# Kernel tuning notes

Hardware: AMD Instinct MI355X
Metric: run time of the kernel (lower is better)

The kernel has to match this reference:

```python
import jax, jax.numpy as jnp
import numpy as np

D_MODEL = 2048
N_HEADS = 16
HEAD_DIM = D_MODEL // N_HEADS
SCALE = HEAD_DIM ** -0.5
LN_EPS = 1e-5
N_LAYERS = 24


def _layernorm(x, g, b):
    mu = jnp.mean(x, axis=-1, keepdims=True)
    var = jnp.mean(jnp.square(x - mu), axis=-1, keepdims=True)
    return (x - mu) * jax.lax.rsqrt(var + LN_EPS) * g + b


def _split_heads(x):  # [B,S,D] -> [B,H,S,hd]
    B, S, _ = x.shape
    return x.reshape(B, S, N_HEADS, HEAD_DIM).transpose(0, 2, 1, 3)


def setup_inputs() -> dict:
    key = jax.random.key(0)
    ks = jax.random.split(key, 12)
    B, St, Si = 2, 2048, 1024
    std_qkv = D_MODEL ** -0.5
    std_o = (2 * N_LAYERS) ** -0.5
    return {
        "q_text": jax.random.normal(ks[0], (B, St, D_MODEL), jnp.float32),
        "q_image": jax.random.normal(ks[1], (B, Si, D_MODEL), jnp.float32),
        "k_text": jax.random.normal(ks[2], (B, St, D_MODEL), jnp.float32),
        "k_image": jax.random.normal(ks[3], (B, Si, D_MODEL), jnp.float32),
        "Wq": jax.random.normal(ks[4], (D_MODEL, D_MODEL), jnp.float32) * std_qkv,
        "Wk": jax.random.normal(ks[5], (D_MODEL, D_MODEL), jnp.float32) * std_qkv,
        "Wv": jax.random.normal(ks[6], (D_MODEL, D_MODEL), jnp.float32) * std_qkv,
        "Wo": jax.random.normal(ks[7], (D_MODEL, D_MODEL), jnp.float32) * std_o,
        "ln_text_g": jnp.ones((D_MODEL,), jnp.float32),
        "ln_text_b": jnp.zeros((D_MODEL,), jnp.float32),
        "ln_image_g": jnp.ones((D_MODEL,), jnp.float32),
        "ln_image_b": jnp.zeros((D_MODEL,), jnp.float32),
    }


def reference(q_text, q_image, k_text, k_image, Wq, Wk, Wv, Wo,
              ln_text_g, ln_text_b, ln_image_g, ln_image_b):
    # Normalize each key modality once, project to K/V, concat along seq.
    kt = _layernorm(k_text, ln_text_g, ln_text_b)
    ki = _layernorm(k_image, ln_image_g, ln_image_b)
    concat_k = jnp.concatenate([_split_heads(kt @ Wk.T), _split_heads(ki @ Wk.T)], axis=2)
    concat_v = jnp.concatenate([_split_heads(kt @ Wv.T), _split_heads(ki @ Wv.T)], axis=2)

    def attend(q, g, b):
        B, S, _ = q.shape
        qn = _layernorm(q, g, b)
        qh = _split_heads(qn @ Wq.T) * SCALE            # [B,H,Sq,hd]
        scores = jnp.einsum('bhqd,bhkd->bhqk', qh, concat_k)
        attn = jax.nn.softmax(scores.astype(jnp.float32), axis=-1).astype(q.dtype)
        out = jnp.einsum('bhqk,bhkd->bhqd', attn, concat_v)
        out = out.transpose(0, 2, 1, 3).reshape(B, S, D_MODEL)
        return out @ Wo.T

    out_text = attend(q_text, ln_text_g, ln_text_b)
    out_image = attend(q_image, ln_image_g, ln_image_b)
    return (out_text, out_image)
```

## Files before the change

kernel.cpp:

```cpp
#include <hip/hip_runtime.h>

typedef __attribute__((ext_vector_type(8))) short bf16x8;
typedef __attribute__((ext_vector_type(4))) float f32x4;
typedef __attribute__((ext_vector_type(8))) unsigned short u16x8;

#define D_MODEL 2048
#define NH 16
#define HD 128
#define SKV 3072
#define QK_SCALE 0.08838834764831845f
#define LOG2E 1.4426950408889634f
#define DEFER_THR 11.5413f

__device__ __forceinline__ unsigned short f2bf(float f) {
  unsigned int u = __float_as_uint(f);
  u += 0x7fffu + ((u >> 16) & 1u);
  return (unsigned short)(u >> 16);
}
__device__ __forceinline__ float exp2hw(float x) {
  float r; asm("v_exp_f32 %0, %1" : "=v"(r) : "v"(x)); return r;
}
__device__ __forceinline__ unsigned int cvtpk(float lo, float hi) {
  unsigned int r; asm("v_cvt_pk_bf16_f32 %0, %1, %2" : "=v"(r) : "v"(lo), "v"(hi)); return r;
}

typedef __attribute__((address_space(1))) void as1_void;
typedef __attribute__((address_space(3))) void as3_void;
__device__ __forceinline__ void gload_lds16(const void* g, void* l) {
  __builtin_amdgcn_global_load_lds((as1_void*)g, (as3_void*)l, 16, 0, 0);
}

#define MFMA16(a, b, c) __builtin_amdgcn_mfma_f32_16x16x32_bf16((a), (b), (c), 0, 0, 0)

__global__ __launch_bounds__(256) void cvt_w_kernel(
    const float* __restrict__ s0, const float* __restrict__ s1,
    const float* __restrict__ s2, const float* __restrict__ s3,
    unsigned short* __restrict__ dstbase) {
  const int y = blockIdx.y;
  const float* src = (y == 0) ? s0 : (y == 1) ? s1 : (y == 2) ? s2 : s3;
  const float scale = (y == 0) ? (QK_SCALE * LOG2E) : 1.0f;
  unsigned short* dst = dstbase + (size_t)y * 4194304;
  int i = blockIdx.x * 256 + threadIdx.x;
  const float4* s = (const float4*)src + (size_t)i * 2;
  float4 a = s[0], b = s[1];
  u16x8 r;
  r[0] = f2bf(a.x * scale); r[1] = f2bf(a.y * scale);
  r[2] = f2bf(a.z * scale); r[3] = f2bf(a.w * scale);
  r[4] = f2bf(b.x * scale); r[5] = f2bf(b.y * scale);
  r[6] = f2bf(b.z * scale); r[7] = f2bf(b.w * scale);
  *((u16x8*)dst + i) = r;
}

__global__ __launch_bounds__(256) void ln_kernel(
    const float* __restrict__ x, const float* __restrict__ gw,
    const float* __restrict__ bw, unsigned short* __restrict__ out,
    int spb, int orpb, int obase) {
  const int row = blockIdx.x;
  const int t = threadIdx.x;
  const int b = row / spb, s = row - b * spb;
  const float* xr = x + (size_t)row * D_MODEL;
  unsigned short* orow = out + ((size_t)b * orpb + obase + s) * D_MODEL;

  float4 v0 = *(const float4*)(xr + t * 8);
  float4 v1 = *(const float4*)(xr + t * 8 + 4);
  float sum = v0.x + v0.y + v0.z + v0.w + v1.x + v1.y + v1.z + v1.w;
  float sq  = v0.x*v0.x + v0.y*v0.y + v0.z*v0.z + v0.w*v0.w
            + v1.x*v1.x + v1.y*v1.y + v1.z*v1.z + v1.w*v1.w;
#pragma unroll
  for (int o = 32; o > 0; o >>= 1) {
    sum += __shfl_down(sum, o);
    sq  += __shfl_down(sq, o);
  }
  __shared__ float red[8];
  const int wv = t >> 6, l = t & 63;
  if (l == 0) { red[wv] = sum; red[4 + wv] = sq; }
  __syncthreads();
  sum = red[0] + red[1] + red[2] + red[3];
  sq  = red[4] + red[5] + red[6] + red[7];
  const float mu = sum * (1.0f / 2048.0f);
  const float var = sq * (1.0f / 2048.0f) - mu * mu;
  const float rs = rsqrtf(var + 1e-5f);

  float4 g0 = *(const float4*)(gw + t * 8);
  float4 g1 = *(const float4*)(gw + t * 8 + 4);
  float4 b0 = *(const float4*)(bw + t * 8);
  float4 b1 = *(const float4*)(bw + t * 8 + 4);
  u16x8 r;
  r[0] = f2bf((v0.x - mu) * rs * g0.x + b0.x);
  r[1] = f2bf((v0.y - mu) * rs * g0.y + b0.y);
  r[2] = f2bf((v0.z - mu) * rs * g0.z + b0.z);
  r[3] = f2bf((v0.w - mu) * rs * g0.w + b0.w);
  r[4] = f2bf((v1.x - mu) * rs * g1.x + b1.x);
  r[5] = f2bf((v1.y - mu) * rs * g1.y + b1.y);
  r[6] = f2bf((v1.z - mu) * rs * g1.z + b1.z);
  r[7] = f2bf((v1.w - mu) * rs * g1.w + b1.w);
  *(u16x8*)(orow + t * 8) = r;
}

__global__ __launch_bounds__(512, 2) void gemm256r_kernel(
    const unsigned short* __restrict__ Aq, const unsigned short* __restrict__ Akv,
    const unsigned short* __restrict__ Wq, const unsigned short* __restrict__ Wk,
    const unsigned short* __restrict__ Wv,
    void* __restrict__ d0, void* __restrict__ d1,
    void* __restrict__ d2, void* __restrict__ d3, int mode) {
  __shared__ unsigned short lds3[3][16384];

  const int tid = threadIdx.x;
  const int wid = tid >> 6, l = tid & 63;
  const int wm = wid >> 2, wn = wid & 3;
  const int fr = l & 15, fg = l >> 4;
  const int rc = (fg * 8) ^ ((fr & 3) << 3);

  const int cpx = gridDim.x >> 3;
  int wg = ((int)blockIdx.x & 7) * cpx + ((int)blockIdx.x >> 3);

  const unsigned short* A = Aq;
  const unsigned short* W = Wq;
  int emode = mode;
  if (mode == 10) {
    int mat = wg / 192; wg -= mat * 192;
    if (mat == 0)      { emode = 0; }
    else if (mat == 1) { emode = 3; A = Akv; W = Wk; }
    else               { emode = 1; A = Akv; W = Wv; }
  }
  const int bm = wg >> 3, bn = wg & 7;

  const int lr = l >> 2;
  const int gsw = ((l & 3) ^ (lr & 3)) * 8;
  const unsigned short* gaBase = A + (size_t)(bm * 256 + wid * 32 + lr) * 2048 + gsw;
  const unsigned short* gbBase = W + (size_t)(bn * 256 + wid * 32 + lr) * 2048 + gsw;

#define STAGE(buf, kt) do {                                          \
    unsigned short* _da = &lds3[(buf)][wid * 1024];                  \
    unsigned short* _db = &lds3[(buf)][8192 + wid * 1024];           \
    const unsigned short* _sa = gaBase + (size_t)(kt) * 32;          \
    const unsigned short* _sb = gbBase + (size_t)(kt) * 32;          \
    gload_lds16(_sa,             _da);                               \
    gload_lds16(_sa + 16 * 2048, _da + 512);                         \
    gload_lds16(_sb,             _db);                               \
    gload_lds16(_sb + 16 * 2048, _db + 512);                         \
  } while (0)

  f32x4 acc[8][4] = {};
  bf16x8 af[8], bf01[2], bf23[2];

  STAGE(0, 0);
  STAGE(1, 1);
  asm volatile("s_waitcnt vmcnt(4)" ::: "memory");
  __builtin_amdgcn_s_barrier();
#pragma unroll
  for (int mi = 0; mi < 8; ++mi)
    af[mi] = *(const bf16x8*)&lds3[0][(wm * 128 + mi * 16 + fr) * 32 + rc];
#pragma unroll
  for (int ni = 0; ni < 2; ++ni)
    bf01[ni] = *(const bf16x8*)&lds3[0][8192 + (wn * 64 + ni * 16 + fr) * 32 + rc];

  int cur = 0;
  for (int t = 0; t < 64; ++t) {
#pragma unroll
    for (int ni = 0; ni < 2; ++ni)
      bf23[ni] = *(const bf16x8*)&lds3[cur][8192 + (wn * 64 + (ni + 2) * 16 + fr) * 32 + rc];
    if (t < 62) {
      int stg = cur + 2; if (stg >= 3) stg -= 3;
      STAGE(stg, t + 2);
    }

    __builtin_amdgcn_s_setprio(1);
#pragma unroll
    for (int mi = 0; mi < 8; ++mi)
#pragma unroll
      for (int ni = 0; ni < 2; ++ni)
        acc[mi][ni] = MFMA16(af[mi], bf01[ni], acc[mi][ni]);
    __builtin_amdgcn_s_setprio(0);

    __builtin_amdgcn_s_setprio(1);
#pragma unroll
    for (int mi = 0; mi < 8; ++mi)
#pragma unroll
      for (int ni = 0; ni < 2; ++ni)
        acc[mi][ni + 2] = MFMA16(af[mi], bf23[ni], acc[mi][ni + 2]);
    __builtin_amdgcn_s_setprio(0);

    __builtin_amdgcn_sched_barrier(0);
    if (t < 62) {
      asm volatile("s_waitcnt vmcnt(4)" ::: "memory");
      __builtin_amdgcn_s_barrier();
    } else if (t == 62) {
      asm volatile("s_waitcnt vmcnt(0)" ::: "memory");
      __builtin_amdgcn_s_barrier();
    }

    int nxt = cur + 1; if (nxt >= 3) nxt -= 3;
    if (t < 63) {
#pragma unroll
      for (int mi = 0; mi < 8; ++mi)
        af[mi] = *(const bf16x8*)&lds3[nxt][(wm * 128 + mi * 16 + fr) * 32 + rc];
#pragma unroll
      for (int ni = 0; ni < 2; ++ni)
        bf01[ni] = *(const bf16x8*)&lds3[nxt][8192 + (wn * 64 + ni * 16 + fr) * 32 + rc];
    }
    cur = nxt;
  }
#undef STAGE

#pragma unroll
  for (int mi = 0; mi < 8; ++mi) {
    const int row0 = bm * 256 + wm * 128 + mi * 16 + fg * 4;
    if (emode == 1) {
      int b = row0 / 3072, s0 = row0 - b * 3072;
#pragma unroll
      for (int ni = 0; ni < 4; ++ni) {
        int col = bn * 256 + wn * 64 + ni * 16 + fr;
        int hh = col >> 7, d = col & 127;
        size_t bh = (size_t)(b * NH + hh);
        size_t idx = (bh * 128 + d) * (size_t)3072 + ((s0 & ~31) | ((s0 & 31) ^ ((d & 3) << 3)));
        uint2 pk;
        pk.x = cvtpk(acc[mi][ni][0], acc[mi][ni][1]);
        pk.y = cvtpk(acc[mi][ni][2], acc[mi][ni][3]);
        *(uint2*)((unsigned short*)d3 + idx) = pk;
      }
    } else {
#pragma unroll
      for (int r = 0; r < 4; ++r) {
        int row = row0 + r;
#pragma unroll
        for (int ni = 0; ni < 4; ++ni) {
          int col = bn * 256 + wn * 64 + ni * 16 + fr;
          float v = acc[mi][ni][r];
          if (emode == 2) {
            ((float*)d0)[(size_t)row * 2048 + col] = v;
          } else if (emode == 0) {
            int hh = col >> 7, d = col & 127;
            if (row < 4096) {
              int b = row >> 11, s = row & 2047;
              ((unsigned short*)d0)[((size_t)(b * NH + hh) * 2048 + s) * 128 + d] = f2bf(v);
            } else {
              int rr = row - 4096, b = rr >> 10, s = rr & 1023;
              ((unsigned short*)d1)[((size_t)(b * NH + hh) * 1024 + s) * 128 + d] = f2bf(v);
            }
          } else {
            int b = row / 3072, s = row - b * 3072;
            int hh = col >> 7, d = col & 127;
            size_t bh = (size_t)(b * NH + hh);
            ((unsigned short*)d2)[(bh * 3072 + s) * 128 + (d ^ ((s & 7) << 3))] = f2bf(v);
          }
        }
      }
    }
  }
}

__global__ __launch_bounds__(256, 3) void attn_kernel(
    const unsigned short* __restrict__ Qt, const unsigned short* __restrict__ Qi,
    const unsigned short* __restrict__ Kh, const unsigned short* __restrict__ Vt,
    unsigned short* __restrict__ AOt, unsigned short* __restrict__ AOi) {
  __shared__ unsigned short Sh[20480];

  const int lin = blockIdx.x;
  const int w768 = (lin & 7) * 96 + (lin >> 3);
  const int qt24 = w768 % 24;
  const int hb   = w768 / 24;
  const int h = hb & 15, b = hb >> 4;
  const bool is_text = qt24 < 16;
  const int qt = is_text ? qt24 : qt24 - 16;
  const int Sq = is_text ? 2048 : 1024;
  const unsigned short* Qh = is_text ? Qt : Qi;
  unsigned short* AO = is_text ? AOt : AOi;

  const int tid = threadIdx.x;
  const int w = tid >> 6, l = tid & 63;
  const int fr = l & 15, fg = l >> 4;
  const size_t bh = (size_t)(b * NH + h);
  unsigned short* Pw = Sh + 16384 + w * 1024;

  const unsigned short* Qbase = Qh + (bh * Sq + (size_t)qt * 128 + w * 32) * HD;
  bf16x8 qf[2][4];
#pragma unroll
  for (int h2 = 0; h2 < 2; ++h2)
#pragma unroll
    for (int c = 0; c < 4; ++c)
      qf[h2][c] = *(const bf16x8*)(Qbase + (h2 * 16 + fr) * HD + c * 32 + fg * 8);

  f32x4 o[2][8] = {};
  float m[2]    = {-1e30f, -1e30f};
  float lsum[2] = {0.f, 0.f};

  const unsigned short* Kb = Kh + bh * (size_t)SKV * HD;
  const unsigned short* Vb = Vt + bh * (size_t)HD * SKV;

  const int swk = (fr & 7) << 3;
  const int swv = (fr & 3) << 3;

#define STAGE_K(kt, half) do {                                                   \
    unsigned short* _d = Sh + (half) * 4096 + w * 1024;                          \
    const unsigned short* _s = Kb + (size_t)((kt) * 32 + w * 8 + (l >> 4)) * 128 \
                               + (l & 15) * 8;                                   \
    gload_lds16(_s, _d);                                                         \
    gload_lds16(_s + 4 * 128, _d + 512);                                         \
  } while (0)
#define STAGE_V(kt, half) do {                                                   \
    unsigned short* _d = Sh + 8192 + (half) * 4096 + w * 1024;                   \
    const unsigned short* _s = Vb + (size_t)(w * 32 + (l >> 2)) * SKV            \
                               + (kt) * 32 + (l & 3) * 8;                        \
    gload_lds16(_s, _d);                                                         \
    gload_lds16(_s + 16 * SKV, _d + 512);                                        \
  } while (0)

  STAGE_K(0, 0);
  for (int kt = 0; kt < 96; ++kt) {
    const int half = kt & 1;
    STAGE_V(kt, half);
    asm volatile("s_waitcnt vmcnt(2)" ::: "memory");
    __builtin_amdgcn_s_barrier();

    const unsigned short* Ksc = Sh + half * 4096;
    f32x4 sT[2][2] = {};
#pragma unroll
    for (int j = 0; j < 2; ++j) {
      const int krb = (j * 16 + fr) * 128;
#pragma unroll
      for (int c = 0; c < 4; ++c) {
        bf16x8 kf = *(const bf16x8*)&Ksc[krb + ((c * 32 + fg * 8) ^ swk)];
        sT[0][j] = MFMA16(kf, qf[0][c], sT[0][j]);
        sT[1][j] = MFMA16(kf, qf[1][c], sT[1][j]);
      }
    }
    if (kt < 95) STAGE_K(kt + 1, half ^ 1);

#pragma unroll
    for (int h2 = 0; h2 < 2; ++h2) {
      float tm = fmaxf(fmaxf(fmaxf(sT[h2][0][0], sT[h2][0][1]),
                             fmaxf(sT[h2][0][2], sT[h2][0][3])),
                       fmaxf(fmaxf(sT[h2][1][0], sT[h2][1][1]),
                             fmaxf(sT[h2][1][2], sT[h2][1][3])));
      tm = fmaxf(tm, __shfl_xor(tm, 16));
      tm = fmaxf(tm, __shfl_xor(tm, 32));
      if (__any(tm - m[h2] > DEFER_THR)) {
        float mn = fmaxf(m[h2], tm);
        float al = exp2hw(m[h2] - mn);
#pragma unroll
        for (int nt = 0; nt < 8; ++nt) {
          f32x4 t = o[h2][nt];
          t[0] *= al; t[1] *= al; t[2] *= al; t[3] *= al;
          o[h2][nt] = t;
        }
        lsum[h2] *= al;
        m[h2] = mn;
      }
      const float mm = m[h2];
      float p00 = exp2hw(sT[h2][0][0] - mm), p01 = exp2hw(sT[h2][0][1] - mm);
      float p02 = exp2hw(sT[h2][0][2] - mm), p03 = exp2hw(sT[h2][0][3] - mm);
      float p10 = exp2hw(sT[h2][1][0] - mm), p11 = exp2hw(sT[h2][1][1] - mm);
      float p12 = exp2hw(sT[h2][1][2] - mm), p13 = exp2hw(sT[h2][1][3] - mm);
      lsum[h2] += (p00 + p01 + p02 + p03) + (p10 + p11 + p12 + p13);
      unsigned short* prow = &Pw[(h2 * 16 + fr) * 32];
      uint2 w0; w0.x = cvtpk(p00, p01); w0.y = cvtpk(p02, p03);
      uint2 w1; w1.x = cvtpk(p10, p11); w1.y = cvtpk(p12, p13);
      *(uint2*)(prow + ((fg * 4) ^ swv))      = w0;
      *(uint2*)(prow + ((16 + fg * 4) ^ swv)) = w1;
    }

    if (kt < 95) asm volatile("s_waitcnt vmcnt(2)" ::: "memory");
    else         asm volatile("s_waitcnt vmcnt(0)" ::: "memory");
    __builtin_amdgcn_s_barrier();

    asm volatile("s_waitcnt lgkmcnt(0)" ::: "memory");
    __builtin_amdgcn_sched_barrier(0);

    const unsigned short* Vsc = Sh + 8192 + half * 4096;
    bf16x8 pb[2];
#pragma unroll
    for (int h2 = 0; h2 < 2; ++h2)
      pb[h2] = *(const bf16x8*)&Pw[(h2 * 16 + fr) * 32 + ((fg * 8) ^ swv)];
#pragma unroll
    for (int nt = 0; nt < 8; ++nt) {
      bf16x8 vf = *(const bf16x8*)&Vsc[(nt * 16 + fr) * 32 + ((fg * 8) ^ swv)];
      o[0][nt] = MFMA16(vf, pb[0], o[0][nt]);
      o[1][nt] = MFMA16(vf, pb[1], o[1][nt]);
    }
    __builtin_amdgcn_s_barrier();
  }
#undef STAGE_K
#undef STAGE_V

  float inv[2];
#pragma unroll
  for (int h2 = 0; h2 < 2; ++h2) {
    float t = lsum[h2];
    t += __shfl_xor(t, 16);
    t += __shfl_xor(t, 32);
    inv[h2] = 1.0f / t;
  }
  unsigned short* Os = &Sh[w * 4096];
#pragma unroll
  for (int h2 = 0; h2 < 2; ++h2) {
    unsigned short* orow = &Os[(h2 * 16 + fr) * 128];
    const int sw8 = (fr & 7) << 3;
#pragma unroll
    for (int nt = 0; nt < 8; ++nt) {
      uint2 pk;
      pk.x = cvtpk(o[h2][nt][0] * inv[h2], o[h2][nt][1] * inv[h2]);
      pk.y = cvtpk(o[h2][nt][2] * inv[h2], o[h2][nt][3] * inv[h2]);
      *(uint2*)(orow + ((nt * 16 + fg * 4) ^ sw8)) = pk;
    }
  }
  asm volatile("s_waitcnt lgkmcnt(0)" ::: "memory");
  __builtin_amdgcn_sched_barrier(0);
  const int qr4 = l >> 4;
  const int dc = (l & 15) * 8;
  unsigned short* AObase = AO + ((size_t)b * Sq + (size_t)qt * 128 + w * 32) * D_MODEL + h * HD;
#pragma unroll
  for (int g = 0; g < 8; ++g) {
    const int row = g * 4 + qr4;
    bf16x8 v = *reinterpret_cast<const bf16x8*>(&Os[row * 128 + (dc ^ ((row & 7) << 3))]);
    *reinterpret_cast<bf16x8*>(&AObase[(size_t)row * D_MODEL + dc]) = v;
  }
}

extern "C" void kernel_launch(void* const* d_in, const int* in_sizes, int n_in,
                              void* d_out, int out_size, void* d_ws, size_t ws_size,
                              hipStream_t stream) {
  const float* q_text  = (const float*)d_in[0];
  const float* q_image = (const float*)d_in[1];
  const float* k_text  = (const float*)d_in[2];
  const float* k_image = (const float*)d_in[3];
  const float* Wq = (const float*)d_in[4];
  const float* Wk = (const float*)d_in[5];
  const float* Wv = (const float*)d_in[6];
  const float* Wo = (const float*)d_in[7];
  const float* ln_tg = (const float*)d_in[8];
  const float* ln_tb = (const float*)d_in[9];
  const float* ln_ig = (const float*)d_in[10];
  const float* ln_ib = (const float*)d_in[11];

  unsigned short* wq  = (unsigned short*)d_ws;
  unsigned short* wk  = wq  + 4194304;
  unsigned short* wv  = wk  + 4194304;
  unsigned short* wo  = wv  + 4194304;
  unsigned short* xqt = wo  + 4194304;
  unsigned short* xqi = xqt + 8388608;
  unsigned short* xk  = xqi + 4194304;
  unsigned short* qht = xk  + 12582912;
  unsigned short* qhi = qht + 8388608;
  unsigned short* kh  = qhi + 4194304;
  unsigned short* vt  = kh  + 12582912;
  const size_t needed = (size_t)(vt + 12582912 - wq) * 2;
  if (ws_size < needed) return;

  cvt_w_kernel<<<dim3(2048, 4), 256, 0, stream>>>(Wq, Wk, Wv, Wo, wq);

  ln_kernel<<<4096, 256, 0, stream>>>(q_text,  ln_tg, ln_tb, xqt, 2048, 2048, 0);
  ln_kernel<<<2048, 256, 0, stream>>>(q_image, ln_ig, ln_ib, xqi, 1024, 1024, 0);
  ln_kernel<<<4096, 256, 0, stream>>>(k_text,  ln_tg, ln_tb, xk, 2048, 3072, 0);
  ln_kernel<<<2048, 256, 0, stream>>>(k_image, ln_ig, ln_ib, xk, 1024, 3072, 2048);

  gemm256r_kernel<<<576, 512, 0, stream>>>(xqt, xk, wq, wk, wv, qht, qhi, kh, vt, 10);

  attn_kernel<<<768, 256, 0, stream>>>(qht, qhi, kh, vt, xqt, xqi);

  gemm256r_kernel<<<192, 512, 0, stream>>>(xqt, nullptr, wo, nullptr, nullptr,
                                           d_out, nullptr, nullptr, nullptr, 2);
}
```

Measured before the change: 515.1 us.

## Restructure GEMM into 8-phase K=64 double-buffered pipeline and fuse layernorm launches

The 256x256 GEMM moves from a 3-stage K=32 ring buffer to a double-buffered K=64 tile. Each pair of K-tiles is split into eight phases that interleave LDS fragment reads, partial global-to-LDS staging and 16-MFMA blocks, with barriers between phases and a 64-column XOR swizzle. The intent is to overlap global loads with MFMA work at finer grain and halve the number of main-loop iterations. The four layernorm launches are merged into one kernel to cut launch overhead. The extra barriers per iteration may add synchronization stalls.

```diff
diff --git a/kernel.cpp b/kernel.cpp
--- a/kernel.cpp
+++ b/kernel.cpp
@@ -51,18 +51,25 @@
   *((u16x8*)dst + i) = r;
 }
 
-__global__ __launch_bounds__(256) void ln_kernel(
-    const float* __restrict__ x, const float* __restrict__ gw,
-    const float* __restrict__ bw, unsigned short* __restrict__ out,
-    int spb, int orpb, int obase) {
-  const int row = blockIdx.x;
+__global__ __launch_bounds__(256) void ln_all_kernel(
+    const float* __restrict__ qt, const float* __restrict__ qi,
+    const float* __restrict__ ktx, const float* __restrict__ kix,
+    const float* __restrict__ gt, const float* __restrict__ bt,
+    const float* __restrict__ gi, const float* __restrict__ bi,
+    unsigned short* __restrict__ xqt, unsigned short* __restrict__ xqi,
+    unsigned short* __restrict__ xk) {
+  const int rid = blockIdx.x;
   const int t = threadIdx.x;
-  const int b = row / spb, s = row - b * spb;
-  const float* xr = x + (size_t)row * D_MODEL;
-  unsigned short* orow = out + ((size_t)b * orpb + obase + s) * D_MODEL;
-
-  float4 v0 = *(const float4*)(xr + t * 8);
-  float4 v1 = *(const float4*)(xr + t * 8 + 4);
+  const float* src; const float* gw; const float* bw; unsigned short* dst;
+  if (rid < 4096)      { src = qt + (size_t)rid * 2048; gw = gt; bw = bt; dst = xqt + (size_t)rid * 2048; }
+  else if (rid < 6144) { int r = rid - 4096; src = qi + (size_t)r * 2048; gw = gi; bw = bi; dst = xqi + (size_t)r * 2048; }
+  else if (rid < 10240){ int r = rid - 6144; src = ktx + (size_t)r * 2048; gw = gt; bw = bt;
+                         int b = r >> 11, s = r & 2047; dst = xk + ((size_t)b * 3072 + s) * 2048; }
+  else                 { int r = rid - 10240; src = kix + (size_t)r * 2048; gw = gi; bw = bi;
+                         int b = r >> 10, s = r & 1023; dst = xk + ((size_t)b * 3072 + 2048 + s) * 2048; }
+
+  float4 v0 = *(const float4*)(src + t * 8);
+  float4 v1 = *(const float4*)(src + t * 8 + 4);
   float sum = v0.x + v0.y + v0.z + v0.w + v1.x + v1.y + v1.z + v1.w;
   float sq  = v0.x*v0.x + v0.y*v0.y + v0.z*v0.z + v0.w*v0.w
             + v1.x*v1.x + v1.y*v1.y + v1.z*v1.z + v1.w*v1.w;
@@ -94,22 +101,22 @@
   r[5] = f2bf((v1.y - mu) * rs * g1.y + b1.y);
   r[6] = f2bf((v1.z - mu) * rs * g1.z + b1.z);
   r[7] = f2bf((v1.w - mu) * rs * g1.w + b1.w);
-  *(u16x8*)(orow + t * 8) = r;
-}
-
-__global__ __launch_bounds__(512, 2) void gemm256r_kernel(
+  *(u16x8*)(dst + t * 8) = r;
+}
+
+__global__ __launch_bounds__(512, 2) void gemm8p_kernel(
     const unsigned short* __restrict__ Aq, const unsigned short* __restrict__ Akv,
     const unsigned short* __restrict__ Wq, const unsigned short* __restrict__ Wk,
     const unsigned short* __restrict__ Wv,
     void* __restrict__ d0, void* __restrict__ d1,
     void* __restrict__ d2, void* __restrict__ d3, int mode) {
-  __shared__ unsigned short lds3[3][16384];
+  __shared__ unsigned short lds[2][2][16384];
 
   const int tid = threadIdx.x;
   const int wid = tid >> 6, l = tid & 63;
   const int wm = wid >> 2, wn = wid & 3;
   const int fr = l & 15, fg = l >> 4;
-  const int rc = (fg * 8) ^ ((fr & 3) << 3);
+  const int swr = (fr & 7) << 3;
 
   const int cpx = gridDim.x >> 3;
   int wg = ((int)blockIdx.x & 7) * cpx + ((int)blockIdx.x >> 3);
@@ -125,83 +132,109 @@
   }
   const int bm = wg >> 3, bn = wg & 7;
 
-  const int lr = l >> 2;
-  const int gsw = ((l & 3) ^ (lr & 3)) * 8;
-  const unsigned short* gaBase = A + (size_t)(bm * 256 + wid * 32 + lr) * 2048 + gsw;
-  const unsigned short* gbBase = W + (size_t)(bn * 256 + wid * 32 + lr) * 2048 + gsw;
-
-#define STAGE(buf, kt) do {                                          \
-    unsigned short* _da = &lds3[(buf)][wid * 1024];                  \
-    unsigned short* _db = &lds3[(buf)][8192 + wid * 1024];           \
-    const unsigned short* _sa = gaBase + (size_t)(kt) * 32;          \
-    const unsigned short* _sb = gbBase + (size_t)(kt) * 32;          \
-    gload_lds16(_sa,             _da);                               \
-    gload_lds16(_sa + 16 * 2048, _da + 512);                         \
-    gload_lds16(_sb,             _db);                               \
-    gload_lds16(_sb + 16 * 2048, _db + 512);                         \
+  const int lr8 = l >> 3;
+  const int gcol = ((l & 7) ^ lr8) * 8;
+  const unsigned short* gaB = A + (size_t)(bm * 256 + wid * 16 + lr8) * 2048 + gcol;
+  const unsigned short* gbB = W + (size_t)(bn * 256 + wid * 16 + lr8) * 2048 + gcol;
+
+#define STAGE_A(kt, h) do {                                                       \
+    unsigned short* _d = &lds[(kt) & 1][0][(h) * 8192 + wid * 1024];              \
+    const unsigned short* _s = gaB + (size_t)(h) * 128 * 2048 + (size_t)(kt) * 64;\
+    gload_lds16(_s,            _d);                                               \
+    gload_lds16(_s + 8 * 2048, _d + 512);                                         \
   } while (0)
+#define STAGE_B(kt, h) do {                                                       \
+    unsigned short* _d = &lds[(kt) & 1][1][(h) * 8192 + wid * 1024];              \
+    const unsigned short* _s = gbB + (size_t)(h) * 128 * 2048 + (size_t)(kt) * 64;\
+    gload_lds16(_s,            _d);                                               \
+    gload_lds16(_s + 8 * 2048, _d + 512);                                         \
+  } while (0)
+
+#define RD_A(dst, miB, dbf)                                                       \
+  _Pragma("unroll") for (int _m = 0; _m < 4; ++_m)                                \
+  _Pragma("unroll") for (int _k = 0; _k < 2; ++_k)                                \
+    dst[_m][_k] = *(const bf16x8*)&lds[dbf][0][(wm * 128 + ((miB) + _m) * 16 + fr) * 64 + ((_k * 32 + fg * 8) ^ swr)];
+#define RD_B(dst, niB, dbf)                                                       \
+  _Pragma("unroll") for (int _n = 0; _n < 2; ++_n)                                \
+  _Pragma("unroll") for (int _k = 0; _k < 2; ++_k)                                \
+    dst[_n][_k] = *(const bf16x8*)&lds[dbf][1][(wn * 64 + ((niB) + _n) * 16 + fr) * 64 + ((_k * 32 + fg * 8) ^ swr)];
+
+#define MM16(aS, miB, niB) do {                                                   \
+    __builtin_amdgcn_s_setprio(1);                                                \
+    _Pragma("unroll") for (int _m = 0; _m < 4; ++_m)                              \
+    _Pragma("unroll") for (int _n = 0; _n < 2; ++_n)                              \
+    _Pragma("unroll") for (int _k = 0; _k < 2; ++_k)                              \
+      acc[(miB) + _m][(niB) + _n] =                                               \
+        MFMA16(aS[_m][_k], bb[_n][_k], acc[(miB) + _m][(niB) + _n]);              \
+    __builtin_amdgcn_s_setprio(0);                                                \
+  } while (0)
+
+#define BAR __builtin_amdgcn_s_barrier()
+#define LG0 do { asm volatile("s_waitcnt lgkmcnt(0)" ::: "memory");               \
+                 __builtin_amdgcn_sched_barrier(0); } while (0)
 
   f32x4 acc[8][4] = {};
-  bf16x8 af[8], bf01[2], bf23[2];
-
-  STAGE(0, 0);
-  STAGE(1, 1);
+  bf16x8 aLo[4][2], aHi[4][2], bb[2][2];
+
+  STAGE_A(0, 0); STAGE_A(0, 1); STAGE_B(0, 0); STAGE_B(0, 1);
+  STAGE_A(1, 0); STAGE_A(1, 1);
   asm volatile("s_waitcnt vmcnt(4)" ::: "memory");
-  __builtin_amdgcn_s_barrier();
-#pragma unroll
-  for (int mi = 0; mi < 8; ++mi)
-    af[mi] = *(const bf16x8*)&lds3[0][(wm * 128 + mi * 16 + fr) * 32 + rc];
-#pragma unroll
-  for (int ni = 0; ni < 2; ++ni)
-    bf01[ni] = *(const bf16x8*)&lds3[0][8192 + (wn * 64 + ni * 16 + fr) * 32 + rc];
-
-  int cur = 0;
-  for (int t = 0; t < 64; ++t) {
-#pragma unroll
-    for (int ni = 0; ni < 2; ++ni)
-      bf23[ni] = *(const bf16x8*)&lds3[cur][8192 + (wn * 64 + (ni + 2) * 16 + fr) * 32 + rc];
-    if (t < 62) {
-      int stg = cur + 2; if (stg >= 3) stg -= 3;
-      STAGE(stg, t + 2);
-    }
-
-    __builtin_amdgcn_s_setprio(1);
-#pragma unroll
-    for (int mi = 0; mi < 8; ++mi)
-#pragma unroll
-      for (int ni = 0; ni < 2; ++ni)
-        acc[mi][ni] = MFMA16(af[mi], bf01[ni], acc[mi][ni]);
-    __builtin_amdgcn_s_setprio(0);
-
-    __builtin_amdgcn_s_setprio(1);
-#pragma unroll
-    for (int mi = 0; mi < 8; ++mi)
-#pragma unroll
-      for (int ni = 0; ni < 2; ++ni)
-        acc[mi][ni + 2] = MFMA16(af[mi], bf23[ni], acc[mi][ni + 2]);
-    __builtin_amdgcn_s_setprio(0);
-
+  BAR;
+
+  for (int i = 0; i < 16; ++i) {
+    const int kt0 = 2 * i;
+    const bool nl = (i < 15);
+    RD_A(aLo, 0, 0); RD_B(bb, 0, 0);
+    STAGE_B(kt0 + 1, 0);
+    BAR; LG0;
+    MM16(aLo, 0, 0);
+    BAR;
+    RD_A(aHi, 4, 0);
+    STAGE_B(kt0 + 1, 1);
+    BAR; LG0;
+    MM16(aHi, 4, 0);
+    BAR;
+    RD_B(bb, 2, 0);
+    if (nl) STAGE_A(kt0 + 2, 0);
+    BAR; LG0;
+    MM16(aLo, 0, 2);
+    BAR;
+    if (nl) STAGE_A(kt0 + 2, 1);
+    BAR; LG0;
+    MM16(aHi, 4, 2);
     __builtin_amdgcn_sched_barrier(0);
-    if (t < 62) {
-      asm volatile("s_waitcnt vmcnt(4)" ::: "memory");
-      __builtin_amdgcn_s_barrier();
-    } else if (t == 62) {
-      asm volatile("s_waitcnt vmcnt(0)" ::: "memory");
-      __builtin_amdgcn_s_barrier();
-    }
-
-    int nxt = cur + 1; if (nxt >= 3) nxt -= 3;
-    if (t < 63) {
-#pragma unroll
-      for (int mi = 0; mi < 8; ++mi)
-        af[mi] = *(const bf16x8*)&lds3[nxt][(wm * 128 + mi * 16 + fr) * 32 + rc];
-#pragma unroll
-      for (int ni = 0; ni < 2; ++ni)
-        bf01[ni] = *(const bf16x8*)&lds3[nxt][8192 + (wn * 64 + ni * 16 + fr) * 32 + rc];
-    }
-    cur = nxt;
-  }
-#undef STAGE
+    if (nl) asm volatile("s_waitcnt vmcnt(4)" ::: "memory");
+    else    asm volatile("s_waitcnt vmcnt(0)" ::: "memory");
+    BAR;
+    RD_A(aLo, 0, 1); RD_B(bb, 0, 1);
+    if (nl) STAGE_B(kt0 + 2, 0);
+    BAR; LG0;
+    MM16(aLo, 0, 0);
+    BAR;
+    RD_A(aHi, 4, 1);
+    if (nl) STAGE_B(kt0 + 2, 1);
+    BAR; LG0;
+    MM16(aHi, 4, 0);
+    BAR;
+    RD_B(bb, 2, 1);
+    if (nl) STAGE_A(kt0 + 3, 0);
+    BAR; LG0;
+    MM16(aLo, 0, 2);
+    BAR;
+    if (nl) STAGE_A(kt0 + 3, 1);
+    BAR; LG0;
+    MM16(aHi, 4, 2);
+    __builtin_amdgcn_sched_barrier(0);
+    if (nl) asm volatile("s_waitcnt vmcnt(4)" ::: "memory");
+    BAR;
+  }
+#undef STAGE_A
+#undef STAGE_B
+#undef RD_A
+#undef RD_B
+#undef MM16
+#undef BAR
+#undef LG0
 
 #pragma unroll
   for (int mi = 0; mi < 8; ++mi) {
@@ -449,15 +482,14 @@
 
   cvt_w_kernel<<<dim3(2048, 4), 256, 0, stream>>>(Wq, Wk, Wv, Wo, wq);
 
-  ln_kernel<<<4096, 256, 0, stream>>>(q_text,  ln_tg, ln_tb, xqt, 2048, 2048, 0);
-  ln_kernel<<<2048, 256, 0, stream>>>(q_image, ln_ig, ln_ib, xqi, 1024, 1024, 0);
-  ln_kernel<<<4096, 256, 0, stream>>>(k_text,  ln_tg, ln_tb, xk, 2048, 3072, 0);
-  ln_kernel<<<2048, 256, 0, stream>>>(k_image, ln_ig, ln_ib, xk, 1024, 3072, 2048);
-
-  gemm256r_kernel<<<576, 512, 0, stream>>>(xqt, xk, wq, wk, wv, qht, qhi, kh, vt, 10);
+  ln_all_kernel<<<12288, 256, 0, stream>>>(q_text, q_image, k_text, k_image,
+                                           ln_tg, ln_tb, ln_ig, ln_ib,
+                                           xqt, xqi, xk);
+
+  gemm8p_kernel<<<576, 512, 0, stream>>>(xqt, xk, wq, wk, wv, qht, qhi, kh, vt, 10);
 
   attn_kernel<<<768, 256, 0, stream>>>(qht, qhi, kh, vt, xqt, xqi);
 
-  gemm256r_kernel<<<192, 512, 0, stream>>>(xqt, nullptr, wo, nullptr, nullptr,
-                                           d_out, nullptr, nullptr, nullptr, 2);
-}
+  gemm8p_kernel<<<192, 512, 0, stream>>>(xqt, nullptr, wo, nullptr, nullptr,
+                                         d_out, nullptr, nullptr, nullptr, 2);
+}
```

Measured after the change: 496.1 us, median of 2. 3.7% less time.
